# Kernel optimization log

Measured on AMD Instinct MI355X. Metric: run time of the kernel, lower is better.

## Reference

```python
import jax, jax.numpy as jnp
import numpy as np

B, D, H = 512, 1024, 2048          # batch, context_dim, l_hidden
MAX_STEPS = 8                       # config.max_l_steps
ATOL = 0.01                         # config.l_conv_atol
THR = 0.1                           # config.commitment_threshold


def setup_inputs() -> dict:
    key = jax.random.key(0)
    ks = jax.random.split(key, 20)
    mat = lambda k, shp, fi: jax.random.normal(k, shp, jnp.float32) / np.float32(np.sqrt(fi))
    inp = dict(
        enc=jax.random.normal(ks[0], (B, D), jnp.float32),
        static_context=jax.random.normal(ks[1], (B, D), jnp.float32),
        # fresh RWKV state: channel 3 (pp, running max-exponent) = -1e30
        l_state=jnp.zeros((B, H, 5), jnp.float32).at[:, :, 3].set(-1e30),
        initial_drift=0.1 * jax.random.normal(ks[2], (B, D), jnp.float32),
        # l_input_proj: Linear(2*D -> H)
        Win=mat(ks[3], (2 * D, H), 2 * D), b_in=jnp.zeros((H,), jnp.float32),
        # context_drift_proj: Linear(H -> D, bias=False)
        Wdrift=mat(ks[4], (H, D), H),
        # l_to_out: Linear(H -> D)
        Wout=mat(ks[5], (H, D), H), b_out=jnp.zeros((D,), jnp.float32),
        # RWKV cell (v4-style) parameters over hidden dim H
        mix_k=jax.random.uniform(ks[6], (H,), jnp.float32),
        mix_v=jax.random.uniform(ks[7], (H,), jnp.float32),
        mix_r=jax.random.uniform(ks[8], (H,), jnp.float32),
        mix_k2=jax.random.uniform(ks[9], (H,), jnp.float32),
        mix_r2=jax.random.uniform(ks[10], (H,), jnp.float32),
        time_decay=0.5 * jax.random.normal(ks[11], (H,), jnp.float32),
        time_first=0.5 * jax.random.normal(ks[12], (H,), jnp.float32),
        Wk=mat(ks[13], (H, H), H), Wv=mat(ks[14], (H, H), H),
        Wr=mat(ks[15], (H, H), H), Wo=mat(ks[16], (H, H), H),
        Wk2=mat(ks[17], (H, H), H), Wv2=mat(ks[18], (H, H), H),
        Wr2=mat(ks[19], (H, H), H),
    )
    return inp


def _forward(enc, static_context, l_state, initial_drift, Win, b_in, Wdrift, Wout, b_out,
             mix_k, mix_v, mix_r, mix_k2, mix_r2, time_decay, time_first,
             Wk, Wv, Wr, Wo, Wk2, Wv2, Wr2):
    def cell(x, state):
        # RWKV-style linear-attention cell. state: [B,H,5] = (x_prev_tm, aa, bb, pp, x_prev_cm)
        xx, aa, bb, pp, cc = (state[..., i] for i in range(5))
        xk = x * mix_k + xx * (1.0 - mix_k)
        xv = x * mix_v + xx * (1.0 - mix_v)
        xr = x * mix_r + xx * (1.0 - mix_r)
        r = jax.nn.sigmoid(xr @ Wr)
        k = xk @ Wk
        v = xv @ Wv
        ww = time_first + k
        q = jnp.maximum(pp, ww)
        e1 = jnp.exp(pp - q); e2 = jnp.exp(ww - q)
        wkv = (e1 * aa + e2 * v) / (e1 * bb + e2)
        ww2 = pp - jnp.exp(time_decay)
        q2 = jnp.maximum(ww2, k)
        e1b = jnp.exp(ww2 - q2); e2b = jnp.exp(k - q2)
        tm_out = (r * wkv) @ Wo
        # channel-mix half of the cell (state channel 4)
        xk2 = x * mix_k2 + cc * (1.0 - mix_k2)
        xr2 = x * mix_r2 + cc * (1.0 - mix_r2)
        r2 = jax.nn.sigmoid(xr2 @ Wr2)
        kk = jnp.square(jax.nn.relu(xk2 @ Wk2))
        out = tm_out + r2 * (kk @ Wv2)
        new_state = jnp.stack([x, e1b * aa + e2b * v, e1b * bb + e2b, q2, x], axis=-1)
        return out, new_state

    def l_input_of(drift):
        v = jnp.concatenate([enc, static_context + drift], axis=-1) @ Win + b_in
        return jnp.clip(v, -50.0, 50.0)

    def step(carry, _):
        drift, sstate, done, csum, cnt = carry
        li = l_input_of(drift)
        out, ns = cell(li, sstate)
        ns = jnp.clip(ns, -50.0, 50.0)
        delta = jnp.tanh(out @ Wdrift)
        nd = jnp.clip(drift + delta, -5.0, 5.0)
        hinge = jnp.minimum(jax.nn.relu(jnp.mean(jnp.sum(nd * nd, axis=-1)) - THR), 100.0)
        conv = jnp.mean(jnp.abs(delta)) < ATOL
        # freeze all updates once converged (early-exit semantics under jit)
        drift = jnp.where(done, drift, nd)
        sstate = jnp.where(done, sstate, ns)
        csum = jnp.where(done, csum, csum + hinge)
        cnt = jnp.where(done, cnt, cnt + 1.0)
        done = jnp.logical_or(done, conv)
        return (drift, sstate, done, csum, cnt), None

    carry0 = (initial_drift, l_state, jnp.array(False), jnp.float32(0.0), jnp.float32(0.0))
    (drift, _, _, csum, cnt), _ = jax.lax.scan(step, carry0, None, length=MAX_STEPS)

    # final commit step uses the ORIGINAL l_state (not the shadow state)
    li = l_input_of(drift)
    final_out, next_state = cell(li, l_state)
    next_state = jnp.clip(next_state, -50.0, 50.0)
    final_enc = enc + final_out @ Wout + b_out
    commitment = csum / jnp.maximum(cnt, 1.0)
    return final_enc, next_state, commitment, drift


def reference(enc, static_context, l_state, initial_drift, Win, b_in, Wdrift, Wout, b_out,
              mix_k, mix_v, mix_r, mix_k2, mix_r2, time_decay, time_first,
              Wk, Wv, Wr, Wo, Wk2, Wv2, Wr2):
    return _forward(enc, static_context, l_state, initial_drift, Win, b_in, Wdrift, Wout, b_out,
                    mix_k, mix_v, mix_r, mix_k2, mix_r2, time_decay, time_first,
                    Wk, Wv, Wr, Wo, Wk2, Wv2, Wr2)
```

## Files before the change

kernel.cpp:

```cpp
#include <hip/hip_runtime.h>
#include <hip/hip_bf16.h>

#define Bb 512
#define Dd 1024
#define Hh 2048
#define BH_ (Bb*Hh)
#define BD_ (Bb*Dd)

typedef unsigned short u16;
typedef __attribute__((ext_vector_type(8))) short short8;
typedef __attribute__((ext_vector_type(4))) float f32x4;

enum { M_F32 = 0, M_IN, M_SIG, M_SQRELU, M_OUT, M_DRIFT, M_FINAL };

struct GemmP {
    const u16* A[3];
    const u16* W[3];
    void* dst[3];
    int mode[3];
    int M, N, K;
    const int* done;
    const float* bias;
    const float* mk; const float* mv; const float* mr; const float* mk2v; const float* mr2v;
    const float* xx; const float* cc;
    const float* lstate;
    float* liF;
    float* stateOut;
    u16 *o1, *o2, *o3, *o4, *o5;
    const float* f1; const float* f2;
    float* drift; float* accAbs; float* accSq;
    float* scal; int nticket;
    const float* enc; const float* bout; float* dout;
};

__global__ __launch_bounds__(512, 4) void gemm_sk(GemmP p) {
    if (p.done && *(volatile const int*)p.done) return;
    const int z = blockIdx.z;
    const u16* __restrict__ A = p.A[z];
    const u16* __restrict__ W = p.W[z];
    const int Kd = p.K;
    const int m0 = blockIdx.y * 64, n0 = blockIdx.x * 64;

    __shared__ alignas(16) u16 As[64 * 136];
    __shared__ alignas(16) u16 Bs[64 * 136];

    const int t = threadIdx.x;
    const int l = t & 63, w = t >> 6;
    const int lane16 = l & 15, quad = l >> 4;
    const int wq = w & 3, kg = w >> 2;
    const int wm = wq & 1, wn = wq >> 1;
    const int srow = t >> 3, scp = t & 7;

    f32x4 zero = {0.f, 0.f, 0.f, 0.f};
    f32x4 acc[2][2];
    acc[0][0] = zero; acc[0][1] = zero; acc[1][0] = zero; acc[1][1] = zero;

    const u16* ap = A + (size_t)(m0 + srow) * Kd + scp * 8;
    const u16* bp = W + (size_t)(n0 + srow) * Kd + scp * 8;

    uint4 ra0 = *(const uint4*)(const void*)(ap);
    uint4 ra1 = *(const uint4*)(const void*)(ap + 64);
    uint4 rb0 = *(const uint4*)(const void*)(bp);
    uint4 rb1 = *(const uint4*)(const void*)(bp + 64);

    for (int k0 = 0; k0 < Kd; k0 += 128) {
        *(uint4*)(void*)&As[srow * 136 + scp * 8]      = ra0;
        *(uint4*)(void*)&As[srow * 136 + scp * 8 + 64] = ra1;
        *(uint4*)(void*)&Bs[srow * 136 + scp * 8]      = rb0;
        *(uint4*)(void*)&Bs[srow * 136 + scp * 8 + 64] = rb1;
        __syncthreads();
        if (k0 + 128 < Kd) {
            ra0 = *(const uint4*)(const void*)(ap + k0 + 128);
            ra1 = *(const uint4*)(const void*)(ap + k0 + 192);
            rb0 = *(const uint4*)(const void*)(bp + k0 + 128);
            rb1 = *(const uint4*)(const void*)(bp + k0 + 192);
        }
        const int kb = kg * 64;
#pragma unroll
        for (int kc = 0; kc < 64; kc += 32) {
            const int col = kb + kc + quad * 8;
            short8 af0 = *(const short8*)(const void*)&As[(wm * 32 + lane16) * 136 + col];
            short8 af1 = *(const short8*)(const void*)&As[(wm * 32 + 16 + lane16) * 136 + col];
            short8 bf0 = *(const short8*)(const void*)&Bs[(wn * 32 + lane16) * 136 + col];
            short8 bf1 = *(const short8*)(const void*)&Bs[(wn * 32 + 16 + lane16) * 136 + col];
            acc[0][0] = __builtin_amdgcn_mfma_f32_16x16x32_bf16(af0, bf0, acc[0][0], 0, 0, 0);
            acc[0][1] = __builtin_amdgcn_mfma_f32_16x16x32_bf16(af0, bf1, acc[0][1], 0, 0, 0);
            acc[1][0] = __builtin_amdgcn_mfma_f32_16x16x32_bf16(af1, bf0, acc[1][0], 0, 0, 0);
            acc[1][1] = __builtin_amdgcn_mfma_f32_16x16x32_bf16(af1, bf1, acc[1][1], 0, 0, 0);
        }
        __syncthreads();
    }

    float* red = (float*)As;
    const int rbase = wq * 1088 + l * 17;
    if (kg == 1) {
#pragma unroll
        for (int sm = 0; sm < 2; ++sm)
#pragma unroll
            for (int sn = 0; sn < 2; ++sn)
#pragma unroll
                for (int i = 0; i < 4; ++i)
                    red[rbase + (sm * 2 + sn) * 4 + i] = acc[sm][sn][i];
    }
    __syncthreads();
    if (kg == 0) {
#pragma unroll
        for (int sm = 0; sm < 2; ++sm)
#pragma unroll
            for (int sn = 0; sn < 2; ++sn)
#pragma unroll
                for (int i = 0; i < 4; ++i)
                    acc[sm][sn][i] += red[rbase + (sm * 2 + sn) * 4 + i];
    }

    const int mode = p.mode[z];
    float sabs = 0.f, ssq = 0.f;
    if (kg == 0) {
#pragma unroll
        for (int sm = 0; sm < 2; ++sm)
#pragma unroll
            for (int sn = 0; sn < 2; ++sn)
#pragma unroll
                for (int i = 0; i < 4; ++i) {
                    const int m = m0 + wm * 32 + sm * 16 + quad * 4 + i;
                    const int n = n0 + wn * 32 + sn * 16 + lane16;
                    const size_t idx = (size_t)m * p.N + n;
                    const float v = acc[sm][sn][i];
                    if (mode == M_F32) {
                        ((float*)p.dst[z])[idx] = v;
                    } else if (mode == M_IN) {
                        float li = fminf(fmaxf(v + p.bias[n], -50.f), 50.f);
                        float xxv, ccv;
                        if (p.lstate) { xxv = p.lstate[idx * 5 + 0]; ccv = p.lstate[idx * 5 + 4]; }
                        else { xxv = p.xx[idx]; ccv = p.cc[idx]; }
                        float mk = p.mk[n], mv = p.mv[n], mr = p.mr[n], mk2 = p.mk2v[n], mr2 = p.mr2v[n];
                        ((__hip_bfloat16*)p.o1)[idx] = __float2bfloat16(li * mk + xxv * (1.f - mk));
                        ((__hip_bfloat16*)p.o2)[idx] = __float2bfloat16(li * mv + xxv * (1.f - mv));
                        ((__hip_bfloat16*)p.o3)[idx] = __float2bfloat16(li * mr + xxv * (1.f - mr));
                        ((__hip_bfloat16*)p.o4)[idx] = __float2bfloat16(li * mk2 + ccv * (1.f - mk2));
                        ((__hip_bfloat16*)p.o5)[idx] = __float2bfloat16(li * mr2 + ccv * (1.f - mr2));
                        if (p.lstate) { p.stateOut[idx * 5 + 0] = li; p.stateOut[idx * 5 + 4] = li; }
                        else p.liF[idx] = li;
                    } else if (mode == M_SIG) {
                        ((float*)p.dst[z])[idx] = 1.f / (1.f + __expf(-v));
                    } else if (mode == M_SQRELU) {
                        float r = fmaxf(v, 0.f);
                        ((__hip_bfloat16*)p.dst[z])[idx] = __float2bfloat16(r * r);
                    } else if (mode == M_OUT) {
                        ((__hip_bfloat16*)p.dst[z])[idx] = __float2bfloat16(p.f1[idx] + p.f2[idx] * v);
                    } else if (mode == M_DRIFT) {
                        float d = tanhf(v);
                        float nd = fminf(fmaxf(p.drift[idx] + d, -5.f), 5.f);
                        p.drift[idx] = nd;
                        sabs += fabsf(d);
                        ssq += nd * nd;
                    } else {
                        p.dout[idx] = p.enc[idx] + v + p.bout[n];
                    }
                }
    }
    if (mode == M_DRIFT) {
        if (kg == 0) {
#pragma unroll
            for (int off = 32; off > 0; off >>= 1) {
                sabs += __shfl_down(sabs, off, 64);
                ssq += __shfl_down(ssq, off, 64);
            }
            if (l == 0) { atomicAdd(p.accAbs, sabs); atomicAdd(p.accSq, ssq); }
        }
        __syncthreads();
        if (t == 0) {
            __threadfence();
            int v = atomicAdd((int*)(p.scal + 5), 1);
            if (v == p.nticket - 1) {
                volatile float* s = p.scal;
                float hinge = fminf(fmaxf(s[4] / (float)Bb - 0.1f, 0.f), 100.f);
                s[1] = s[1] + hinge;
                s[2] = s[2] + 1.f;
                if (s[3] / (float)BD_ < 0.01f) ((volatile int*)p.scal)[0] = 1;
                s[3] = 0.f; s[4] = 0.f;
                ((volatile int*)p.scal)[5] = 0;
            }
        }
    }
}

__global__ void transposeW(const float* __restrict__ src, u16* __restrict__ dst, int K, int N) {
    __shared__ float tile[32][33];
    int kt = blockIdx.y * 32, nt = blockIdx.x * 32;
    int tx = threadIdx.x, ty = threadIdx.y;
#pragma unroll
    for (int j = 0; j < 4; j++)
        tile[ty + j * 8][tx] = src[(size_t)(kt + ty + j * 8) * N + nt + tx];
    __syncthreads();
    __hip_bfloat16* d = (__hip_bfloat16*)dst;
#pragma unroll
    for (int j = 0; j < 4; j++)
        d[(size_t)(nt + ty + j * 8) * K + kt + tx] = __float2bfloat16(tile[tx][ty + j * 8]);
}

__global__ void initstate(const float* __restrict__ lstate, const float* __restrict__ idrift,
                          float* xx, float* aa, float* bb, float* pp, float* cc,
                          float* drift, float* scal) {
    int i = blockIdx.x * 256 + threadIdx.x;
    if (i < BH_) {
        const float* s = lstate + (size_t)i * 5;
        xx[i] = s[0]; aa[i] = s[1]; bb[i] = s[2]; pp[i] = s[3]; cc[i] = s[4];
    }
    if (i < BD_) drift[i] = idrift[i];
    if (i == 0) {
        ((int*)scal)[0] = 0; scal[1] = 0.f; scal[2] = 0.f; scal[3] = 0.f; scal[4] = 0.f;
        ((int*)scal)[5] = 0;
    }
}

__global__ void prep(const float* __restrict__ enc, const float* __restrict__ sc,
                     const float* __restrict__ drift, u16* __restrict__ Acat, const int* done) {
    if (done && *(volatile const int*)done) return;
    int i = blockIdx.x * 256 + threadIdx.x;
    if (i >= BD_) return;
    int m = i >> 10, d = i & 1023;
    __hip_bfloat16* Ab = (__hip_bfloat16*)Acat;
    Ab[(size_t)m * 2048 + d] = __float2bfloat16(enc[i]);
    Ab[(size_t)m * 2048 + 1024 + d] = __float2bfloat16(sc[i] + drift[i]);
}

__global__ void mix1(const float* __restrict__ Kp, const float* __restrict__ Vp,
                     const float* __restrict__ Rp,
                     float* aa, float* bb, float* pp, float* xx, float* cc,
                     const float* __restrict__ Li,
                     const float* __restrict__ tf, const float* __restrict__ td,
                     u16* __restrict__ rwkv,
                     const float* __restrict__ lstate, float* stateOut,
                     const int* done) {
    if (done && *(volatile const int*)done) return;
    int i = blockIdx.x * 256 + threadIdx.x;
    if (i >= BH_) return;
    int h = i & (Hh - 1);
    float k = Kp[i], v = Vp[i], rpre = Rp[i];
    float a, b, P;
    if (lstate) { a = lstate[(size_t)i * 5 + 1]; b = lstate[(size_t)i * 5 + 2]; P = lstate[(size_t)i * 5 + 3]; }
    else { a = aa[i]; b = bb[i]; P = pp[i]; }
    float r = 1.f / (1.f + __expf(-rpre));
    float ww = tf[h] + k;
    float q = fmaxf(P, ww);
    float e1 = __expf(P - q), e2 = __expf(ww - q);
    float wkv = (e1 * a + e2 * v) / (e1 * b + e2);
    ((__hip_bfloat16*)rwkv)[i] = __float2bfloat16(r * wkv);
    float ww2 = P - __expf(td[h]);
    float q2 = fmaxf(ww2, k);
    float e1b = __expf(ww2 - q2), e2b = __expf(k - q2);
    float na = fminf(fmaxf(e1b * a + e2b * v, -50.f), 50.f);
    float nb = fminf(fmaxf(e1b * b + e2b, -50.f), 50.f);
    float nq = fminf(fmaxf(q2, -50.f), 50.f);
    if (lstate) {
        stateOut[(size_t)i * 5 + 1] = na; stateOut[(size_t)i * 5 + 2] = nb; stateOut[(size_t)i * 5 + 3] = nq;
    } else {
        aa[i] = na; bb[i] = nb; pp[i] = nq;
        float li = Li[i];
        xx[i] = li; cc[i] = li;
    }
}

__global__ void tailk(const float* __restrict__ scal, const float* __restrict__ drift, float* __restrict__ dout) {
    int i = blockIdx.x * 256 + threadIdx.x;
    const size_t OC = (size_t)BD_ + (size_t)5 * BH_;
    if (i == 0) dout[OC] = scal[1] / fmaxf(scal[2], 1.f);
    if (i < BD_) dout[OC + 1 + i] = drift[i];
}

extern "C" void kernel_launch(void* const* d_in, const int* in_sizes, int n_in,
                              void* d_out, int out_size, void* d_ws, size_t ws_size,
                              hipStream_t stream) {
    const float* enc    = (const float*)d_in[0];
    const float* sc     = (const float*)d_in[1];
    const float* lstate = (const float*)d_in[2];
    const float* idrift = (const float*)d_in[3];
    const float* Win    = (const float*)d_in[4];
    const float* b_in   = (const float*)d_in[5];
    const float* Wdrift = (const float*)d_in[6];
    const float* Wout   = (const float*)d_in[7];
    const float* b_out  = (const float*)d_in[8];
    const float* mix_k  = (const float*)d_in[9];
    const float* mix_v  = (const float*)d_in[10];
    const float* mix_r  = (const float*)d_in[11];
    const float* mix_k2 = (const float*)d_in[12];
    const float* mix_r2 = (const float*)d_in[13];
    const float* tdec   = (const float*)d_in[14];
    const float* tfirst = (const float*)d_in[15];
    const float* Wk  = (const float*)d_in[16];
    const float* Wv  = (const float*)d_in[17];
    const float* Wr  = (const float*)d_in[18];
    const float* Wo  = (const float*)d_in[19];
    const float* Wk2 = (const float*)d_in[20];
    const float* Wv2 = (const float*)d_in[21];
    const float* Wr2 = (const float*)d_in[22];
    float* dout = (float*)d_out;

    const size_t BHs = (size_t)Bb * Hh;
    const size_t BDs = (size_t)Bb * Dd;

    const size_t need_f32 = 9 * BHs + BDs + 16;
    const size_t need_u16 = (size_t)2 * Dd * Hh + 7 * (size_t)Hh * Hh + 2 * (size_t)Hh * Dd + 8 * BHs;
    const size_t need_bytes = need_f32 * 4 + need_u16 * 2;
    if (ws_size < need_bytes) return;

    float* f = (float*)d_ws;
    float* xx  = f;
    float* aa  = xx + BHs;
    float* bbp = aa + BHs;
    float* ppp = bbp + BHs;
    float* cc  = ppp + BHs;
    float* Li  = cc + BHs;
    float* Kp  = Li + BHs;
    float* Vp  = Kp + BHs;
    float* Rp  = Vp + BHs;
    float* Tm  = Kp;
    float* R2  = Vp;
    float* drift = Rp + BHs;
    float* scal  = drift + BDs;
    u16* u = (u16*)(scal + 16);
    u16* WinT  = u; u += (size_t)2 * Dd * Hh;
    u16* WkT   = u; u += (size_t)Hh * Hh;
    u16* WvT   = u; u += (size_t)Hh * Hh;
    u16* WrT   = u; u += (size_t)Hh * Hh;
    u16* WoT   = u; u += (size_t)Hh * Hh;
    u16* Wk2T  = u; u += (size_t)Hh * Hh;
    u16* Wv2T  = u; u += (size_t)Hh * Hh;
    u16* Wr2T  = u; u += (size_t)Hh * Hh;
    u16* WdT   = u; u += (size_t)Hh * Dd;
    u16* WoutT = u; u += (size_t)Hh * Dd;
    u16* Acat = u; u += BHs;
    u16* Xk   = u; u += BHs;
    u16* Xv   = u; u += BHs;
    u16* Xr   = u; u += BHs;
    u16* Xk2  = u; u += BHs;
    u16* Xr2  = u; u += BHs;
    u16* Rw   = u; u += BHs;
    u16* Kk   = u; u += BHs;
    u16* Ob   = Acat;

    int* doneptr = (int*)scal;
    float* accAbs = scal + 3;
    float* accSq  = scal + 4;

    dim3 tb(32, 8);
    transposeW<<<dim3(Hh / 32, (2 * Dd) / 32), tb, 0, stream>>>(Win, WinT, 2 * Dd, Hh);
    transposeW<<<dim3(Hh / 32, Hh / 32), tb, 0, stream>>>(Wk,  WkT,  Hh, Hh);
    transposeW<<<dim3(Hh / 32, Hh / 32), tb, 0, stream>>>(Wv,  WvT,  Hh, Hh);
    transposeW<<<dim3(Hh / 32, Hh / 32), tb, 0, stream>>>(Wr,  WrT,  Hh, Hh);
    transposeW<<<dim3(Hh / 32, Hh / 32), tb, 0, stream>>>(Wo,  WoT,  Hh, Hh);
    transposeW<<<dim3(Hh / 32, Hh / 32), tb, 0, stream>>>(Wk2, Wk2T, Hh, Hh);
    transposeW<<<dim3(Hh / 32, Hh / 32), tb, 0, stream>>>(Wv2, Wv2T, Hh, Hh);
    transposeW<<<dim3(Hh / 32, Hh / 32), tb, 0, stream>>>(Wr2, Wr2T, Hh, Hh);
    transposeW<<<dim3(Dd / 32, Hh / 32), tb, 0, stream>>>(Wdrift, WdT, Hh, Dd);
    transposeW<<<dim3(Dd / 32, Hh / 32), tb, 0, stream>>>(Wout, WoutT, Hh, Dd);

    initstate<<<(BH_ + 255) / 256, 256, 0, stream>>>(lstate, idrift, xx, aa, bbp, ppp, cc, drift, scal);

    GemmP p1 = {};
    p1.A[0] = Acat; p1.W[0] = WinT; p1.mode[0] = M_IN;
    p1.M = Bb; p1.N = Hh; p1.K = 2 * Dd;
    p1.done = doneptr;
    p1.bias = b_in; p1.mk = mix_k; p1.mv = mix_v; p1.mr = mix_r; p1.mk2v = mix_k2; p1.mr2v = mix_r2;
    p1.xx = xx; p1.cc = cc; p1.liF = Li;
    p1.o1 = Xk; p1.o2 = Xv; p1.o3 = Xr; p1.o4 = Xk2; p1.o5 = Xr2;

    GemmP p2 = {};
    p2.A[0] = Xk; p2.A[1] = Xv; p2.A[2] = Xr;
    p2.W[0] = WkT; p2.W[1] = WvT; p2.W[2] = WrT;
    p2.mode[0] = M_F32; p2.mode[1] = M_F32; p2.mode[2] = M_F32;
    p2.dst[0] = Kp; p2.dst[1] = Vp; p2.dst[2] = Rp;
    p2.M = Bb; p2.N = Hh; p2.K = Hh;
    p2.done = doneptr;

    GemmP p3 = {};
    p3.A[0] = Rw; p3.A[1] = Xr2; p3.A[2] = Xk2;
    p3.W[0] = WoT; p3.W[1] = Wr2T; p3.W[2] = Wk2T;
    p3.mode[0] = M_F32; p3.mode[1] = M_SIG; p3.mode[2] = M_SQRELU;
    p3.dst[0] = Tm; p3.dst[1] = R2; p3.dst[2] = Kk;
    p3.M = Bb; p3.N = Hh; p3.K = Hh;
    p3.done = doneptr;

    GemmP p4 = {};
    p4.A[0] = Kk; p4.W[0] = Wv2T; p4.mode[0] = M_OUT; p4.dst[0] = Ob;
    p4.M = Bb; p4.N = Hh; p4.K = Hh;
    p4.f1 = Tm; p4.f2 = R2;
    p4.done = doneptr;

    GemmP p5 = {};
    p5.A[0] = Ob; p5.W[0] = WdT; p5.mode[0] = M_DRIFT;
    p5.M = Bb; p5.N = Dd; p5.K = Hh;
    p5.drift = drift; p5.accAbs = accAbs; p5.accSq = accSq;
    p5.scal = scal; p5.nticket = (Dd / 64) * (Bb / 64);
    p5.done = doneptr;

    dim3 gH(Hh / 64, Bb / 64, 1);
    dim3 gH3(Hh / 64, Bb / 64, 3);
    dim3 gD(Dd / 64, Bb / 64, 1);

    for (int s = 0; s < 8; ++s) {
        prep<<<(BD_ + 255) / 256, 256, 0, stream>>>(enc, sc, drift, Acat, doneptr);
        gemm_sk<<<gH, 512, 0, stream>>>(p1);
        gemm_sk<<<gH3, 512, 0, stream>>>(p2);
        mix1<<<(BH_ + 255) / 256, 256, 0, stream>>>(Kp, Vp, Rp, aa, bbp, ppp, xx, cc, Li,
                                                    tfirst, tdec, Rw, nullptr, nullptr, doneptr);
        gemm_sk<<<gH3, 512, 0, stream>>>(p3);
        gemm_sk<<<gH, 512, 0, stream>>>(p4);
        gemm_sk<<<gD, 512, 0, stream>>>(p5);
    }

    float* stateOut = dout + BD_;

    prep<<<(BD_ + 255) / 256, 256, 0, stream>>>(enc, sc, drift, Acat, nullptr);

    GemmP f1p = p1;
    f1p.done = nullptr; f1p.lstate = lstate; f1p.stateOut = stateOut;
    gemm_sk<<<gH, 512, 0, stream>>>(f1p);

    GemmP f2p = p2; f2p.done = nullptr;
    gemm_sk<<<gH3, 512, 0, stream>>>(f2p);

    mix1<<<(BH_ + 255) / 256, 256, 0, stream>>>(Kp, Vp, Rp, aa, bbp, ppp, xx, cc, Li,
                                                tfirst, tdec, Rw, lstate, stateOut, nullptr);

    GemmP f3p = p3; f3p.done = nullptr;
    gemm_sk<<<gH3, 512, 0, stream>>>(f3p);

    GemmP f4p = p4; f4p.done = nullptr;
    gemm_sk<<<gH, 512, 0, stream>>>(f4p);

    GemmP f5p = {};
    f5p.A[0] = Ob; f5p.W[0] = WoutT; f5p.mode[0] = M_FINAL;
    f5p.M = Bb; f5p.N = Dd; f5p.K = Hh;
    f5p.enc = enc; f5p.bout = b_out; f5p.dout = dout;
    gemm_sk<<<gD, 512, 0, stream>>>(f5p);

    tailk<<<(BD_ + 255) / 256, 256, 0, stream>>>(scal, drift, dout);
}
```

Measured before the change: 1.682 ms.

## Rework GEMM pipeline with async LDS loads, swizzle, and fused elementwise stages

```diff
diff --git a/kernel.cpp b/kernel.cpp
--- a/kernel.cpp
+++ b/kernel.cpp
@@ -11,29 +11,40 @@
 typedef __attribute__((ext_vector_type(8))) short short8;
 typedef __attribute__((ext_vector_type(4))) float f32x4;
 
-enum { M_F32 = 0, M_IN, M_SIG, M_SQRELU, M_OUT, M_DRIFT, M_FINAL };
+enum { M_F32 = 0, M_IN, M_SIG, M_SQRELU, M_MIX, M_OB, M_DRIFT, M_FINAL };
 
 struct GemmP {
-    const u16* A[3];
-    const u16* W[3];
-    void* dst[3];
-    int mode[3];
+    const u16* A[5];
+    const u16* W[5];
+    void* dst[5];
+    int mode[5];
     int M, N, K;
     const int* done;
     const float* bias;
     const float* mk; const float* mv; const float* mr; const float* mk2v; const float* mr2v;
-    const float* xx; const float* cc;
+    float* xx; float* cc;
     const float* lstate;
     float* liF;
     float* stateOut;
     u16 *o1, *o2, *o3, *o4, *o5;
-    const float* f1; const float* f2;
+    const float* Kp; const float* Vp; const float* Rp;
+    float* aa; float* bbp; float* ppp;
+    const float* Li;
+    const float* tf; const float* td;
+    u16* Rw;
+    const float* R2; float* V2;
+    const float* V2r;
     float* drift; float* accAbs; float* accSq;
     float* scal; int nticket;
     const float* enc; const float* bout; float* dout;
+    const float* sc; u16* acat;
 };
 
-__global__ __launch_bounds__(512, 4) void gemm_sk(GemmP p) {
+#define GLDS16(gp, lp) __builtin_amdgcn_global_load_lds( \
+    (const __attribute__((address_space(1))) void*)(gp), \
+    (__attribute__((address_space(3))) void*)(lp), 16, 0, 0)
+
+__global__ __launch_bounds__(256, 5) void gemm_sk(GemmP p) {
     if (p.done && *(volatile const int*)p.done) return;
     const int z = blockIdx.z;
     const u16* __restrict__ A = p.A[z];
@@ -41,138 +52,142 @@
     const int Kd = p.K;
     const int m0 = blockIdx.y * 64, n0 = blockIdx.x * 64;
 
-    __shared__ alignas(16) u16 As[64 * 136];
-    __shared__ alignas(16) u16 Bs[64 * 136];
+    __shared__ alignas(16) u16 smem[4][64 * 64];
 
     const int t = threadIdx.x;
     const int l = t & 63, w = t >> 6;
     const int lane16 = l & 15, quad = l >> 4;
-    const int wq = w & 3, kg = w >> 2;
-    const int wm = wq & 1, wn = wq >> 1;
-    const int srow = t >> 3, scp = t & 7;
+    const int wm = w & 1, wn = w >> 1;
+    const int r8 = l >> 3, c8 = l & 7;
+    const int cs = c8 ^ r8;
+
+    const u16* ag0 = A + (size_t)(m0 + 8 * w + r8) * Kd + cs * 8;
+    const u16* ag1 = A + (size_t)(m0 + 8 * (w + 4) + r8) * Kd + cs * 8;
+    const u16* bg0 = W + (size_t)(n0 + 8 * w + r8) * Kd + cs * 8;
+    const u16* bg1 = W + (size_t)(n0 + 8 * (w + 4) + r8) * Kd + cs * 8;
 
     f32x4 zero = {0.f, 0.f, 0.f, 0.f};
     f32x4 acc[2][2];
     acc[0][0] = zero; acc[0][1] = zero; acc[1][0] = zero; acc[1][1] = zero;
 
-    const u16* ap = A + (size_t)(m0 + srow) * Kd + scp * 8;
-    const u16* bp = W + (size_t)(n0 + srow) * Kd + scp * 8;
-
-    uint4 ra0 = *(const uint4*)(const void*)(ap);
-    uint4 ra1 = *(const uint4*)(const void*)(ap + 64);
-    uint4 rb0 = *(const uint4*)(const void*)(bp);
-    uint4 rb1 = *(const uint4*)(const void*)(bp + 64);
-
-    for (int k0 = 0; k0 < Kd; k0 += 128) {
-        *(uint4*)(void*)&As[srow * 136 + scp * 8]      = ra0;
-        *(uint4*)(void*)&As[srow * 136 + scp * 8 + 64] = ra1;
-        *(uint4*)(void*)&Bs[srow * 136 + scp * 8]      = rb0;
-        *(uint4*)(void*)&Bs[srow * 136 + scp * 8 + 64] = rb1;
-        __syncthreads();
-        if (k0 + 128 < Kd) {
-            ra0 = *(const uint4*)(const void*)(ap + k0 + 128);
-            ra1 = *(const uint4*)(const void*)(ap + k0 + 192);
-            rb0 = *(const uint4*)(const void*)(bp + k0 + 128);
-            rb1 = *(const uint4*)(const void*)(bp + k0 + 192);
+    GLDS16(ag0, &smem[0][512 * w]);
+    GLDS16(ag1, &smem[0][512 * (w + 4)]);
+    GLDS16(bg0, &smem[2][512 * w]);
+    GLDS16(bg1, &smem[2][512 * (w + 4)]);
+    __syncthreads();
+
+    int buf = 0;
+    for (int k0 = 0; k0 < Kd; k0 += 64) {
+        if (k0 + 64 < Kd) {
+            const int nb = buf ^ 1;
+            GLDS16(ag0 + k0 + 64, &smem[nb][512 * w]);
+            GLDS16(ag1 + k0 + 64, &smem[nb][512 * (w + 4)]);
+            GLDS16(bg0 + k0 + 64, &smem[2 + nb][512 * w]);
+            GLDS16(bg1 + k0 + 64, &smem[2 + nb][512 * (w + 4)]);
         }
-        const int kb = kg * 64;
-#pragma unroll
-        for (int kc = 0; kc < 64; kc += 32) {
-            const int col = kb + kc + quad * 8;
-            short8 af0 = *(const short8*)(const void*)&As[(wm * 32 + lane16) * 136 + col];
-            short8 af1 = *(const short8*)(const void*)&As[(wm * 32 + 16 + lane16) * 136 + col];
-            short8 bf0 = *(const short8*)(const void*)&Bs[(wn * 32 + lane16) * 136 + col];
-            short8 bf1 = *(const short8*)(const void*)&Bs[(wn * 32 + 16 + lane16) * 136 + col];
+        const u16* As = smem[buf];
+        const u16* Bs = smem[2 + buf];
+#pragma unroll
+        for (int kc = 0; kc < 2; ++kc) {
+            const int cg = kc * 4 + quad;
+            const int ra0 = wm * 32 + lane16, ra1 = ra0 + 16;
+            const int rb0 = wn * 32 + lane16, rb1 = rb0 + 16;
+            short8 af0 = *(const short8*)(const void*)&As[ra0 * 64 + ((cg ^ (ra0 & 7)) << 3)];
+            short8 af1 = *(const short8*)(const void*)&As[ra1 * 64 + ((cg ^ (ra1 & 7)) << 3)];
+            short8 bf0 = *(const short8*)(const void*)&Bs[rb0 * 64 + ((cg ^ (rb0 & 7)) << 3)];
+            short8 bf1 = *(const short8*)(const void*)&Bs[rb1 * 64 + ((cg ^ (rb1 & 7)) << 3)];
             acc[0][0] = __builtin_amdgcn_mfma_f32_16x16x32_bf16(af0, bf0, acc[0][0], 0, 0, 0);
             acc[0][1] = __builtin_amdgcn_mfma_f32_16x16x32_bf16(af0, bf1, acc[0][1], 0, 0, 0);
             acc[1][0] = __builtin_amdgcn_mfma_f32_16x16x32_bf16(af1, bf0, acc[1][0], 0, 0, 0);
             acc[1][1] = __builtin_amdgcn_mfma_f32_16x16x32_bf16(af1, bf1, acc[1][1], 0, 0, 0);
         }
         __syncthreads();
-    }
-
-    float* red = (float*)As;
-    const int rbase = wq * 1088 + l * 17;
-    if (kg == 1) {
-#pragma unroll
-        for (int sm = 0; sm < 2; ++sm)
-#pragma unroll
-            for (int sn = 0; sn < 2; ++sn)
-#pragma unroll
-                for (int i = 0; i < 4; ++i)
-                    red[rbase + (sm * 2 + sn) * 4 + i] = acc[sm][sn][i];
-    }
-    __syncthreads();
-    if (kg == 0) {
-#pragma unroll
-        for (int sm = 0; sm < 2; ++sm)
-#pragma unroll
-            for (int sn = 0; sn < 2; ++sn)
-#pragma unroll
-                for (int i = 0; i < 4; ++i)
-                    acc[sm][sn][i] += red[rbase + (sm * 2 + sn) * 4 + i];
+        buf ^= 1;
     }
 
     const int mode = p.mode[z];
     float sabs = 0.f, ssq = 0.f;
-    if (kg == 0) {
-#pragma unroll
-        for (int sm = 0; sm < 2; ++sm)
-#pragma unroll
-            for (int sn = 0; sn < 2; ++sn)
-#pragma unroll
-                for (int i = 0; i < 4; ++i) {
-                    const int m = m0 + wm * 32 + sm * 16 + quad * 4 + i;
-                    const int n = n0 + wn * 32 + sn * 16 + lane16;
-                    const size_t idx = (size_t)m * p.N + n;
-                    const float v = acc[sm][sn][i];
-                    if (mode == M_F32) {
-                        ((float*)p.dst[z])[idx] = v;
-                    } else if (mode == M_IN) {
-                        float li = fminf(fmaxf(v + p.bias[n], -50.f), 50.f);
-                        float xxv, ccv;
-                        if (p.lstate) { xxv = p.lstate[idx * 5 + 0]; ccv = p.lstate[idx * 5 + 4]; }
-                        else { xxv = p.xx[idx]; ccv = p.cc[idx]; }
-                        float mk = p.mk[n], mv = p.mv[n], mr = p.mr[n], mk2 = p.mk2v[n], mr2 = p.mr2v[n];
-                        ((__hip_bfloat16*)p.o1)[idx] = __float2bfloat16(li * mk + xxv * (1.f - mk));
-                        ((__hip_bfloat16*)p.o2)[idx] = __float2bfloat16(li * mv + xxv * (1.f - mv));
-                        ((__hip_bfloat16*)p.o3)[idx] = __float2bfloat16(li * mr + xxv * (1.f - mr));
-                        ((__hip_bfloat16*)p.o4)[idx] = __float2bfloat16(li * mk2 + ccv * (1.f - mk2));
-                        ((__hip_bfloat16*)p.o5)[idx] = __float2bfloat16(li * mr2 + ccv * (1.f - mr2));
-                        if (p.lstate) { p.stateOut[idx * 5 + 0] = li; p.stateOut[idx * 5 + 4] = li; }
-                        else p.liF[idx] = li;
-                    } else if (mode == M_SIG) {
-                        ((float*)p.dst[z])[idx] = 1.f / (1.f + __expf(-v));
-                    } else if (mode == M_SQRELU) {
-                        float r = fmaxf(v, 0.f);
-                        ((__hip_bfloat16*)p.dst[z])[idx] = __float2bfloat16(r * r);
-                    } else if (mode == M_OUT) {
-                        ((__hip_bfloat16*)p.dst[z])[idx] = __float2bfloat16(p.f1[idx] + p.f2[idx] * v);
-                    } else if (mode == M_DRIFT) {
-                        float d = tanhf(v);
-                        float nd = fminf(fmaxf(p.drift[idx] + d, -5.f), 5.f);
-                        p.drift[idx] = nd;
-                        sabs += fabsf(d);
-                        ssq += nd * nd;
+#pragma unroll
+    for (int sm = 0; sm < 2; ++sm)
+#pragma unroll
+        for (int sn = 0; sn < 2; ++sn)
+#pragma unroll
+            for (int i = 0; i < 4; ++i) {
+                const int m = m0 + wm * 32 + sm * 16 + quad * 4 + i;
+                const int n = n0 + wn * 32 + sn * 16 + lane16;
+                const size_t idx = (size_t)m * p.N + n;
+                const float v = acc[sm][sn][i];
+                if (mode == M_F32) {
+                    ((float*)p.dst[z])[idx] = v;
+                } else if (mode == M_IN) {
+                    float li = fminf(fmaxf(v + p.bias[n], -50.f), 50.f);
+                    float xxv, ccv;
+                    if (p.lstate) { xxv = p.lstate[idx * 5 + 0]; ccv = p.lstate[idx * 5 + 4]; }
+                    else { xxv = p.xx[idx]; ccv = p.cc[idx]; }
+                    float mk = p.mk[n], mv = p.mv[n], mr = p.mr[n], mk2 = p.mk2v[n], mr2 = p.mr2v[n];
+                    ((__hip_bfloat16*)p.o1)[idx] = __float2bfloat16(li * mk + xxv * (1.f - mk));
+                    ((__hip_bfloat16*)p.o2)[idx] = __float2bfloat16(li * mv + xxv * (1.f - mv));
+                    ((__hip_bfloat16*)p.o3)[idx] = __float2bfloat16(li * mr + xxv * (1.f - mr));
+                    ((__hip_bfloat16*)p.o4)[idx] = __float2bfloat16(li * mk2 + ccv * (1.f - mk2));
+                    ((__hip_bfloat16*)p.o5)[idx] = __float2bfloat16(li * mr2 + ccv * (1.f - mr2));
+                    if (p.lstate) { p.stateOut[idx * 5 + 0] = li; p.stateOut[idx * 5 + 4] = li; }
+                    else p.liF[idx] = li;
+                } else if (mode == M_SIG) {
+                    ((float*)p.dst[z])[idx] = 1.f / (1.f + __expf(-v));
+                } else if (mode == M_SQRELU) {
+                    float r = fmaxf(v, 0.f);
+                    ((__hip_bfloat16*)p.dst[z])[idx] = __float2bfloat16(r * r);
+                } else if (mode == M_MIX) {
+                    float k = p.Kp[idx], vv = p.Vp[idx], rpre = p.Rp[idx];
+                    float a, b, P;
+                    if (p.lstate) { a = p.lstate[idx * 5 + 1]; b = p.lstate[idx * 5 + 2]; P = p.lstate[idx * 5 + 3]; }
+                    else { a = p.aa[idx]; b = p.bbp[idx]; P = p.ppp[idx]; }
+                    float r = 1.f / (1.f + __expf(-rpre));
+                    float ww = p.tf[n] + k;
+                    float q = fmaxf(P, ww);
+                    float e1 = __expf(P - q), e2 = __expf(ww - q);
+                    float wkv = (e1 * a + e2 * vv) / (e1 * b + e2);
+                    ((__hip_bfloat16*)p.Rw)[idx] = __float2bfloat16(r * wkv);
+                    float ww2 = P - __expf(p.td[n]);
+                    float q2 = fmaxf(ww2, k);
+                    float e1b = __expf(ww2 - q2), e2b = __expf(k - q2);
+                    float na  = fminf(fmaxf(e1b * a + e2b * vv, -50.f), 50.f);
+                    float nb2 = fminf(fmaxf(e1b * b + e2b, -50.f), 50.f);
+                    float nq  = fminf(fmaxf(q2, -50.f), 50.f);
+                    if (p.lstate) {
+                        p.stateOut[idx * 5 + 1] = na; p.stateOut[idx * 5 + 2] = nb2; p.stateOut[idx * 5 + 3] = nq;
                     } else {
-                        p.dout[idx] = p.enc[idx] + v + p.bout[n];
+                        p.aa[idx] = na; p.bbp[idx] = nb2; p.ppp[idx] = nq;
+                        float li = p.Li[idx];
+                        p.xx[idx] = li; p.cc[idx] = li;
                     }
+                    p.V2[idx] = p.R2[idx] * v;
+                } else if (mode == M_OB) {
+                    ((__hip_bfloat16*)p.dst[z])[idx] = __float2bfloat16(v + p.V2r[idx]);
+                } else if (mode == M_DRIFT) {
+                    float d = tanhf(v);
+                    float nd = fminf(fmaxf(p.drift[idx] + d, -5.f), 5.f);
+                    p.drift[idx] = nd;
+                    ((__hip_bfloat16*)p.acat)[(size_t)m * 2048 + 1024 + n] = __float2bfloat16(p.sc[idx] + nd);
+                    sabs += fabsf(d);
+                    ssq += nd * nd;
+                } else {
+                    p.dout[idx] = p.enc[idx] + v + p.bout[n];
                 }
-    }
+            }
+
     if (mode == M_DRIFT) {
-        if (kg == 0) {
-#pragma unroll
-            for (int off = 32; off > 0; off >>= 1) {
-                sabs += __shfl_down(sabs, off, 64);
-                ssq += __shfl_down(ssq, off, 64);
-            }
-            if (l == 0) { atomicAdd(p.accAbs, sabs); atomicAdd(p.accSq, ssq); }
+#pragma unroll
+        for (int off = 32; off > 0; off >>= 1) {
+            sabs += __shfl_down(sabs, off, 64);
+            ssq += __shfl_down(ssq, off, 64);
         }
+        if (l == 0) { atomicAdd(p.accAbs, sabs); atomicAdd(p.accSq, ssq); }
         __syncthreads();
         if (t == 0) {
             __threadfence();
-            int v = atomicAdd((int*)(p.scal + 5), 1);
-            if (v == p.nticket - 1) {
+            int vtk = atomicAdd((int*)(p.scal + 5), 1);
+            if (vtk == p.nticket - 1) {
                 volatile float* s = p.scal;
                 float hinge = fminf(fmaxf(s[4] / (float)Bb - 0.1f, 0.f), 100.f);
                 s[1] = s[1] + hinge;
@@ -185,80 +200,43 @@
     }
 }
 
-__global__ void transposeW(const float* __restrict__ src, u16* __restrict__ dst, int K, int N) {
+struct TP { const float* src[7]; u16* dst[7]; int K; int N; };
+
+__global__ void transposeWz(TP tp) {
     __shared__ float tile[32][33];
+    const float* __restrict__ src = tp.src[blockIdx.z];
+    u16* __restrict__ dst = tp.dst[blockIdx.z];
     int kt = blockIdx.y * 32, nt = blockIdx.x * 32;
     int tx = threadIdx.x, ty = threadIdx.y;
 #pragma unroll
     for (int j = 0; j < 4; j++)
-        tile[ty + j * 8][tx] = src[(size_t)(kt + ty + j * 8) * N + nt + tx];
+        tile[ty + j * 8][tx] = src[(size_t)(kt + ty + j * 8) * tp.N + nt + tx];
     __syncthreads();
     __hip_bfloat16* d = (__hip_bfloat16*)dst;
 #pragma unroll
     for (int j = 0; j < 4; j++)
-        d[(size_t)(nt + ty + j * 8) * K + kt + tx] = __float2bfloat16(tile[tx][ty + j * 8]);
+        d[(size_t)(nt + ty + j * 8) * tp.K + kt + tx] = __float2bfloat16(tile[tx][ty + j * 8]);
 }
 
 __global__ void initstate(const float* __restrict__ lstate, const float* __restrict__ idrift,
+                          const float* __restrict__ enc, const float* __restrict__ sc,
                           float* xx, float* aa, float* bb, float* pp, float* cc,
-                          float* drift, float* scal) {
+                          float* drift, float* scal, u16* acat) {
     int i = blockIdx.x * 256 + threadIdx.x;
     if (i < BH_) {
         const float* s = lstate + (size_t)i * 5;
         xx[i] = s[0]; aa[i] = s[1]; bb[i] = s[2]; pp[i] = s[3]; cc[i] = s[4];
     }
-    if (i < BD_) drift[i] = idrift[i];
+    if (i < BD_) {
+        drift[i] = idrift[i];
+        int m = i >> 10, d = i & 1023;
+        __hip_bfloat16* Ab = (__hip_bfloat16*)acat;
+        Ab[(size_t)m * 2048 + d] = __float2bfloat16(enc[i]);
+        Ab[(size_t)m * 2048 + 1024 + d] = __float2bfloat16(sc[i] + idrift[i]);
+    }
     if (i == 0) {
         ((int*)scal)[0] = 0; scal[1] = 0.f; scal[2] = 0.f; scal[3] = 0.f; scal[4] = 0.f;
         ((int*)scal)[5] = 0;
-    }
-}
-
-__global__ void prep(const float* __restrict__ enc, const float* __restrict__ sc,
-                     const float* __restrict__ drift, u16* __restrict__ Acat, const int* done) {
-    if (done && *(volatile const int*)done) return;
-    int i = blockIdx.x * 256 + threadIdx.x;
-    if (i >= BD_) return;
-    int m = i >> 10, d = i & 1023;
-    __hip_bfloat16* Ab = (__hip_bfloat16*)Acat;
-    Ab[(size_t)m * 2048 + d] = __float2bfloat16(enc[i]);
-    Ab[(size_t)m * 2048 + 1024 + d] = __float2bfloat16(sc[i] + drift[i]);
-}
-
-__global__ void mix1(const float* __restrict__ Kp, const float* __restrict__ Vp,
-                     const float* __restrict__ Rp,
-                     float* aa, float* bb, float* pp, float* xx, float* cc,
-                     const float* __restrict__ Li,
-                     const float* __restrict__ tf, const float* __restrict__ td,
-                     u16* __restrict__ rwkv,
-                     const float* __restrict__ lstate, float* stateOut,
-                     const int* done) {
-    if (done && *(volatile const int*)done) return;
-    int i = blockIdx.x * 256 + threadIdx.x;
-    if (i >= BH_) return;
-    int h = i & (Hh - 1);
-    float k = Kp[i], v = Vp[i], rpre = Rp[i];
-    float a, b, P;
-    if (lstate) { a = lstate[(size_t)i * 5 + 1]; b = lstate[(size_t)i * 5 + 2]; P = lstate[(size_t)i * 5 + 3]; }
-    else { a = aa[i]; b = bb[i]; P = pp[i]; }
-    float r = 1.f / (1.f + __expf(-rpre));
-    float ww = tf[h] + k;
-    float q = fmaxf(P, ww);
-    float e1 = __expf(P - q), e2 = __expf(ww - q);
-    float wkv = (e1 * a + e2 * v) / (e1 * b + e2);
-    ((__hip_bfloat16*)rwkv)[i] = __float2bfloat16(r * wkv);
-    float ww2 = P - __expf(td[h]);
-    float q2 = fmaxf(ww2, k);
-    float e1b = __expf(ww2 - q2), e2b = __expf(k - q2);
-    float na = fminf(fmaxf(e1b * a + e2b * v, -50.f), 50.f);
-    float nb = fminf(fmaxf(e1b * b + e2b, -50.f), 50.f);
-    float nq = fminf(fmaxf(q2, -50.f), 50.f);
-    if (lstate) {
-        stateOut[(size_t)i * 5 + 1] = na; stateOut[(size_t)i * 5 + 2] = nb; stateOut[(size_t)i * 5 + 3] = nq;
-    } else {
-        aa[i] = na; bb[i] = nb; pp[i] = nq;
-        float li = Li[i];
-        xx[i] = li; cc[i] = li;
     }
 }
 
@@ -300,8 +278,8 @@
     const size_t BHs = (size_t)Bb * Hh;
     const size_t BDs = (size_t)Bb * Dd;
 
-    const size_t need_f32 = 9 * BHs + BDs + 16;
-    const size_t need_u16 = (size_t)2 * Dd * Hh + 7 * (size_t)Hh * Hh + 2 * (size_t)Hh * Dd + 8 * BHs;
+    const size_t need_f32 = 10 * BHs + BDs + 16;
+    const size_t need_u16 = (size_t)2 * Dd * Hh + 7 * (size_t)Hh * Hh + 2 * (size_t)Hh * Dd + 9 * BHs;
     const size_t need_bytes = need_f32 * 4 + need_u16 * 2;
     if (ws_size < need_bytes) return;
 
@@ -315,10 +293,10 @@
     float* Kp  = Li + BHs;
     float* Vp  = Kp + BHs;
     float* Rp  = Vp + BHs;
-    float* Tm  = Kp;
-    float* R2  = Vp;
-    float* drift = Rp + BHs;
+    float* R2  = Rp + BHs;
+    float* drift = R2 + BHs;
     float* scal  = drift + BDs;
+    float* V2 = Kp;
     u16* u = (u16*)(scal + 16);
     u16* WinT  = u; u += (size_t)2 * Dd * Hh;
     u16* WkT   = u; u += (size_t)Hh * Hh;
@@ -338,103 +316,109 @@
     u16* Xr2  = u; u += BHs;
     u16* Rw   = u; u += BHs;
     u16* Kk   = u; u += BHs;
-    u16* Ob   = Acat;
+    u16* Ob   = u; u += BHs;
 
     int* doneptr = (int*)scal;
     float* accAbs = scal + 3;
     float* accSq  = scal + 4;
 
     dim3 tb(32, 8);
-    transposeW<<<dim3(Hh / 32, (2 * Dd) / 32), tb, 0, stream>>>(Win, WinT, 2 * Dd, Hh);
-    transposeW<<<dim3(Hh / 32, Hh / 32), tb, 0, stream>>>(Wk,  WkT,  Hh, Hh);
-    transposeW<<<dim3(Hh / 32, Hh / 32), tb, 0, stream>>>(Wv,  WvT,  Hh, Hh);
-    transposeW<<<dim3(Hh / 32, Hh / 32), tb, 0, stream>>>(Wr,  WrT,  Hh, Hh);
-    transposeW<<<dim3(Hh / 32, Hh / 32), tb, 0, stream>>>(Wo,  WoT,  Hh, Hh);
-    transposeW<<<dim3(Hh / 32, Hh / 32), tb, 0, stream>>>(Wk2, Wk2T, Hh, Hh);
-    transposeW<<<dim3(Hh / 32, Hh / 32), tb, 0, stream>>>(Wv2, Wv2T, Hh, Hh);
-    transposeW<<<dim3(Hh / 32, Hh / 32), tb, 0, stream>>>(Wr2, Wr2T, Hh, Hh);
-    transposeW<<<dim3(Dd / 32, Hh / 32), tb, 0, stream>>>(Wdrift, WdT, Hh, Dd);
-    transposeW<<<dim3(Dd / 32, Hh / 32), tb, 0, stream>>>(Wout, WoutT, Hh, Dd);
-
-    initstate<<<(BH_ + 255) / 256, 256, 0, stream>>>(lstate, idrift, xx, aa, bbp, ppp, cc, drift, scal);
-
-    GemmP p1 = {};
-    p1.A[0] = Acat; p1.W[0] = WinT; p1.mode[0] = M_IN;
-    p1.M = Bb; p1.N = Hh; p1.K = 2 * Dd;
-    p1.done = doneptr;
-    p1.bias = b_in; p1.mk = mix_k; p1.mv = mix_v; p1.mr = mix_r; p1.mk2v = mix_k2; p1.mr2v = mix_r2;
-    p1.xx = xx; p1.cc = cc; p1.liF = Li;
-    p1.o1 = Xk; p1.o2 = Xv; p1.o3 = Xr; p1.o4 = Xk2; p1.o5 = Xr2;
-
-    GemmP p2 = {};
-    p2.A[0] = Xk; p2.A[1] = Xv; p2.A[2] = Xr;
-    p2.W[0] = WkT; p2.W[1] = WvT; p2.W[2] = WrT;
-    p2.mode[0] = M_F32; p2.mode[1] = M_F32; p2.mode[2] = M_F32;
-    p2.dst[0] = Kp; p2.dst[1] = Vp; p2.dst[2] = Rp;
-    p2.M = Bb; p2.N = Hh; p2.K = Hh;
-    p2.done = doneptr;
-
-    GemmP p3 = {};
-    p3.A[0] = Rw; p3.A[1] = Xr2; p3.A[2] = Xk2;
-    p3.W[0] = WoT; p3.W[1] = Wr2T; p3.W[2] = Wk2T;
-    p3.mode[0] = M_F32; p3.mode[1] = M_SIG; p3.mode[2] = M_SQRELU;
-    p3.dst[0] = Tm; p3.dst[1] = R2; p3.dst[2] = Kk;
-    p3.M = Bb; p3.N = Hh; p3.K = Hh;
-    p3.done = doneptr;
-
-    GemmP p4 = {};
-    p4.A[0] = Kk; p4.W[0] = Wv2T; p4.mode[0] = M_OUT; p4.dst[0] = Ob;
-    p4.M = Bb; p4.N = Hh; p4.K = Hh;
-    p4.f1 = Tm; p4.f2 = R2;
-    p4.done = doneptr;
-
-    GemmP p5 = {};
-    p5.A[0] = Ob; p5.W[0] = WdT; p5.mode[0] = M_DRIFT;
-    p5.M = Bb; p5.N = Dd; p5.K = Hh;
-    p5.drift = drift; p5.accAbs = accAbs; p5.accSq = accSq;
-    p5.scal = scal; p5.nticket = (Dd / 64) * (Bb / 64);
-    p5.done = doneptr;
+    TP tpa = {};
+    tpa.src[0] = Wk;  tpa.dst[0] = WkT;
+    tpa.src[1] = Wv;  tpa.dst[1] = WvT;
+    tpa.src[2] = Wr;  tpa.dst[2] = WrT;
+    tpa.src[3] = Wo;  tpa.dst[3] = WoT;
+    tpa.src[4] = Wk2; tpa.dst[4] = Wk2T;
+    tpa.src[5] = Wv2; tpa.dst[5] = Wv2T;
+    tpa.src[6] = Wr2; tpa.dst[6] = Wr2T;
+    tpa.K = Hh; tpa.N = Hh;
+    transposeWz<<<dim3(Hh / 32, Hh / 32, 7), tb, 0, stream>>>(tpa);
+    TP tpb = {};
+    tpb.src[0] = Win; tpb.dst[0] = WinT; tpb.K = 2 * Dd; tpb.N = Hh;
+    transposeWz<<<dim3(Hh / 32, (2 * Dd) / 32, 1), tb, 0, stream>>>(tpb);
+    TP tpc = {};
+    tpc.src[0] = Wdrift; tpc.dst[0] = WdT;
+    tpc.src[1] = Wout;   tpc.dst[1] = WoutT;
+    tpc.K = Hh; tpc.N = Dd;
+    transposeWz<<<dim3(Dd / 32, Hh / 32, 2), tb, 0, stream>>>(tpc);
+
+    initstate<<<(BH_ + 255) / 256, 256, 0, stream>>>(lstate, idrift, enc, sc,
+                                                     xx, aa, bbp, ppp, cc, drift, scal, Acat);
+
+    GemmP g1 = {};
+    g1.A[0] = Acat; g1.W[0] = WinT; g1.mode[0] = M_IN;
+    g1.M = Bb; g1.N = Hh; g1.K = 2 * Dd;
+    g1.done = doneptr;
+    g1.bias = b_in; g1.mk = mix_k; g1.mv = mix_v; g1.mr = mix_r; g1.mk2v = mix_k2; g1.mr2v = mix_r2;
+    g1.xx = xx; g1.cc = cc; g1.liF = Li;
+    g1.o1 = Xk; g1.o2 = Xv; g1.o3 = Xr; g1.o4 = Xk2; g1.o5 = Xr2;
+
+    GemmP g2 = {};
+    g2.A[0] = Xk;  g2.W[0] = WkT;  g2.mode[0] = M_F32;    g2.dst[0] = Kp;
+    g2.A[1] = Xv;  g2.W[1] = WvT;  g2.mode[1] = M_F32;    g2.dst[1] = Vp;
+    g2.A[2] = Xr;  g2.W[2] = WrT;  g2.mode[2] = M_F32;    g2.dst[2] = Rp;
+    g2.A[3] = Xr2; g2.W[3] = Wr2T; g2.mode[3] = M_SIG;    g2.dst[3] = R2;
+    g2.A[4] = Xk2; g2.W[4] = Wk2T; g2.mode[4] = M_SQRELU; g2.dst[4] = Kk;
+    g2.M = Bb; g2.N = Hh; g2.K = Hh;
+    g2.done = doneptr;
+
+    GemmP g2b = {};
+    g2b.A[0] = Kk; g2b.W[0] = Wv2T; g2b.mode[0] = M_MIX;
+    g2b.M = Bb; g2b.N = Hh; g2b.K = Hh;
+    g2b.done = doneptr;
+    g2b.Kp = Kp; g2b.Vp = Vp; g2b.Rp = Rp;
+    g2b.aa = aa; g2b.bbp = bbp; g2b.ppp = ppp;
+    g2b.xx = xx; g2b.cc = cc; g2b.Li = Li;
+    g2b.tf = tfirst; g2b.td = tdec;
+    g2b.Rw = Rw; g2b.R2 = R2; g2b.V2 = V2;
+
+    GemmP g3 = {};
+    g3.A[0] = Rw; g3.W[0] = WoT; g3.mode[0] = M_OB; g3.dst[0] = Ob;
+    g3.M = Bb; g3.N = Hh; g3.K = Hh;
+    g3.done = doneptr;
+    g3.V2r = V2;
+
+    GemmP g5 = {};
+    g5.A[0] = Ob; g5.W[0] = WdT; g5.mode[0] = M_DRIFT;
+    g5.M = Bb; g5.N = Dd; g5.K = Hh;
+    g5.done = doneptr;
+    g5.drift = drift; g5.accAbs = accAbs; g5.accSq = accSq;
+    g5.scal = scal; g5.nticket = (Dd / 64) * (Bb / 64);
+    g5.sc = sc; g5.acat = Acat;
 
     dim3 gH(Hh / 64, Bb / 64, 1);
-    dim3 gH3(Hh / 64, Bb / 64, 3);
+    dim3 gH5(Hh / 64, Bb / 64, 5);
     dim3 gD(Dd / 64, Bb / 64, 1);
 
     for (int s = 0; s < 8; ++s) {
-        prep<<<(BD_ + 255) / 256, 256, 0, stream>>>(enc, sc, drift, Acat, doneptr);
-        gemm_sk<<<gH, 512, 0, stream>>>(p1);
-        gemm_sk<<<gH3, 512, 0, stream>>>(p2);
-        mix1<<<(BH_ + 255) / 256, 256, 0, stream>>>(Kp, Vp, Rp, aa, bbp, ppp, xx, cc, Li,
-                                                    tfirst, tdec, Rw, nullptr, nullptr, doneptr);
-        gemm_sk<<<gH3, 512, 0, stream>>>(p3);
-        gemm_sk<<<gH, 512, 0, stream>>>(p4);
-        gemm_sk<<<gD, 512, 0, stream>>>(p5);
+        gemm_sk<<<gH,  256, 0, stream>>>(g1);
+        gemm_sk<<<gH5, 256, 0, stream>>>(g2);
+        gemm_sk<<<gH,  256, 0, stream>>>(g2b);
+        gemm_sk<<<gH,  256, 0, stream>>>(g3);
+        gemm_sk<<<gD,  256, 0, stream>>>(g5);
     }
 
     float* stateOut = dout + BD_;
 
-    prep<<<(BD_ + 255) / 256, 256, 0, stream>>>(enc, sc, drift, Acat, nullptr);
-
-    GemmP f1p = p1;
+    GemmP f1p = g1;
     f1p.done = nullptr; f1p.lstate = lstate; f1p.stateOut = stateOut;
-    gemm_sk<<<gH, 512, 0, stream>>>(f1p);
-
-    GemmP f2p = p2; f2p.done = nullptr;
-    gemm_sk<<<gH3, 512, 0, stream>>>(f2p);
-
-    mix1<<<(BH_ + 255) / 256, 256, 0, stream>>>(Kp, Vp, Rp, aa, bbp, ppp, xx, cc, Li,
-                                                tfirst, tdec, Rw, lstate, stateOut, nullptr);
-
-    GemmP f3p = p3; f3p.done = nullptr;
-    gemm_sk<<<gH3, 512, 0, stream>>>(f3p);
-
-    GemmP f4p = p4; f4p.done = nullptr;
-    gemm_sk<<<gH, 512, 0, stream>>>(f4p);
+    gemm_sk<<<gH, 256, 0, stream>>>(f1p);
+
+    GemmP f2p = g2; f2p.done = nullptr;
+    gemm_sk<<<gH5, 256, 0, stream>>>(f2p);
+
+    GemmP f2bp = g2b;
+    f2bp.done = nullptr; f2bp.lstate = lstate; f2bp.stateOut = stateOut;
+    gemm_sk<<<gH, 256, 0, stream>>>(f2bp);
+
+    GemmP f3p = g3; f3p.done = nullptr;
+    gemm_sk<<<gH, 256, 0, stream>>>(f3p);
 
     GemmP f5p = {};
     f5p.A[0] = Ob; f5p.W[0] = WoutT; f5p.mode[0] = M_FINAL;
     f5p.M = Bb; f5p.N = Dd; f5p.K = Hh;
     f5p.enc = enc; f5p.bout = b_out; f5p.dout = dout;
-    gemm_sk<<<gD, 512, 0, stream>>>(f5p);
+    gemm_sk<<<gD, 256, 0, stream>>>(f5p);
 
     tailk<<<(BD_ + 255) / 256, 256, 0, stream>>>(scal, drift, dout);
 }
```

Measured after the change: 2.038 ms. 1.21x slower.
